# Kernel optimization log

Measured on AMD Instinct MI355X. Metric: run time of the kernel, lower is better.

Reference implementation:

```python
import jax, jax.numpy as jnp
import numpy as np

S = 100                     # MC weight samples
B = 128                     # batch
CONV1 = (100, 20, 1, 5, 5)  # (S, Cout, Cin, kh, kw)
CONV2 = (100, 50, 20, 5, 5)
AFF1 = (100, 500, 800)      # (S, out, in)
AFF2 = (100, 10, 500)
W_OFF = np.cumsum([0, 500, 25000, 400000, 5000])
B_OFF = np.cumsum([0, 20, 50, 500, 10])
NW, NB = 430500, 580


def _softplus(r):
    return jnp.log1p(jnp.exp(r))  # sigma_T(rho) = log(1 + exp(rho))


def _conv(h, w, b):
    # h: (B, S or 1, Cin, H, W); w: (S, Cout, Cin, kh, kw); b: (S, Cout)
    def one(xs, ws):  # xs: (B,Cin,H,W), ws: (Cout,Cin,kh,kw)
        return jax.lax.conv_general_dilated(xs, ws, (1, 1), 'VALID')
    if h.shape[1] == 1:  # shared input broadcast over samples (first layer)
        out = jax.vmap(one, in_axes=(None, 0), out_axes=1)(h[:, 0], w)
    else:
        out = jax.vmap(one, in_axes=(1, 0), out_axes=1)(h, w)
    return out + b[None, :, :, None, None]  # (B,S,Cout,H',W')


def _maxpool(h):  # 2x2 stride-2 over trailing spatial dims
    return jax.lax.reduce_window(h, -jnp.inf, jax.lax.max,
                                 (1, 1, 1, 2, 2), (1, 1, 1, 2, 2), 'VALID')


def setup_inputs() -> dict:
    key = jax.random.key(0)
    ks = jax.random.split(key, 4)
    x = jax.random.normal(ks[0], (B, 1, 28, 28), dtype=jnp.float32)
    e = jax.random.normal(ks[1], (S, NW + NB), dtype=jnp.float32)
    mu_w = jax.random.normal(ks[2], (NW,), dtype=jnp.float32) * 0.05
    rho_w = jnp.ones((NW,), dtype=jnp.float32) * 0.5
    mu_b = jax.random.normal(ks[3], (NB,), dtype=jnp.float32) * 0.05
    rho_b = jnp.ones((NB,), dtype=jnp.float32) * 0.5
    return {"x": x, "e": e, "mu_w": mu_w, "rho_w": rho_w,
            "mu_b": mu_b, "rho_b": rho_b}


def reference(x, e, mu_w, rho_w, mu_b, rho_b):
    # reparameterized per-sample weights: (S, NW) and (S, NB)
    w = mu_w + _softplus(rho_w) * e[:, :NW]
    b = mu_b + _softplus(rho_b) * e[:, NW:]

    h = x[:, None]  # (B,1,1,28,28): singleton MC dim broadcasts
    # conv1 + relu + pool
    h = _conv(h, w[:, W_OFF[0]:W_OFF[1]].reshape(CONV1), b[:, B_OFF[0]:B_OFF[1]])
    h = _maxpool(jax.nn.relu(h))                     # (B,S,20,12,12)
    # conv2 + relu + pool
    h = _conv(h, w[:, W_OFF[1]:W_OFF[2]].reshape(CONV2), b[:, B_OFF[1]:B_OFF[2]])
    h = _maxpool(jax.nn.relu(h))                     # (B,S,50,4,4)
    h = h.reshape(h.shape[0], h.shape[1], -1)        # (B,S,800)
    # aff1 + relu
    w3 = w[:, W_OFF[2]:W_OFF[3]].reshape(AFF1)
    h = jax.nn.relu(jnp.einsum('bsi,soi->bso', h, w3) + b[None, :, B_OFF[2]:B_OFF[3]])
    # aff2 + log_softmax
    w4 = w[:, W_OFF[3]:W_OFF[4]].reshape(AFF2)
    h = jnp.einsum('bsi,soi->bso', h, w4) + b[None, :, B_OFF[3]:B_OFF[4]]
    h = jax.nn.log_softmax(h, axis=-1)               # (B,S,10)
    return h.mean(axis=1)                            # eval path: mean over MC samples
```

## Files before the change

kernel.cpp:

```cpp
#include <hip/hip_runtime.h>
#include <math.h>

#define Sn 100
#define Bn 128
#define NWc 430500
#define EWc 431080

typedef __attribute__((ext_vector_type(8)))  short bhalf8;
typedef __attribute__((ext_vector_type(16))) float fx16;

__device__ __forceinline__ float sp_f(float r){
    return fmaxf(r, 0.f) + log1pf(__expf(-fabsf(r)));
}
__device__ __forceinline__ ushort bfr(float f){
    union { float f; uint u; } c; c.f = f;
    uint r = (c.u + 0x7FFFu + ((c.u >> 16) & 1u)) >> 16;
    return (ushort)r;
}

__global__ void k00_sp(const float* __restrict__ rho_w, const float* __restrict__ rho_b,
                       float* __restrict__ sp_all){
    int i = blockIdx.x * blockDim.x + threadIdx.x;
    if (i < NWc)      sp_all[i] = sp_f(rho_w[i]);
    else if (i < EWc) sp_all[i] = sp_f(rho_b[i - NWc]);
}

__global__ void k0_gen(const float* __restrict__ e, const float* __restrict__ mu_w,
                       const float* __restrict__ sp_all, const float* __restrict__ mu_b,
                       float* __restrict__ w1, ushort* __restrict__ w2r,
                       float* __restrict__ w4, float* __restrict__ ball){
    const int per = 31080;
    int idx = blockIdx.x * blockDim.x + threadIdx.x;
    if (idx >= Sn * per) return;
    int s = idx / per, j = idx % per;
    if (j < 500){
        float v = fmaf(sp_all[j], e[s*EWc + j], mu_w[j]);
        w1[s*500 + j] = v;
    } else if (j < 25500){
        int g = j;
        float v = fmaf(sp_all[g], e[s*EWc + g], mu_w[g]);
        int j2 = j - 500;
        int oc = j2 / 500, rem = j2 % 500;
        int ic = rem / 25, kk = rem % 25;
        w2r[s*51200 + (kk*64 + oc)*32 + ic] = bfr(v);
    } else if (j < 30500){
        int g = 425500 + (j - 25500);
        float v = fmaf(sp_all[g], e[s*EWc + g], mu_w[g]);
        w4[s*5000 + (j - 25500)] = v;
    } else {
        int k = j - 30500;
        float v = fmaf(sp_all[NWc + k], e[s*EWc + NWc + k], mu_b[k]);
        ball[s*580 + k] = v;
    }
}

__global__ __launch_bounds__(256, 2) void k1_conv1(const float* __restrict__ x,
        const float* __restrict__ w1, const float* __restrict__ ball,
        ushort* __restrict__ h1p){
    __shared__ __align__(16) float xs[784];
    __shared__ __align__(16) float w1s[500];
    __shared__ float b1s[20];
    __shared__ __align__(16) ushort ots[2880];
    int bid = blockIdx.x;
    int s = bid / Bn, b = bid % Bn;
    int tid = threadIdx.x;
    for (int i = tid; i < 784; i += 256) xs[i] = x[b*784 + i];
    for (int i = tid; i < 500; i += 256) w1s[i] = w1[s*500 + i];
    if (tid < 20) b1s[tid] = ball[s*580 + tid];
    __syncthreads();
    if (tid < 240){
        int c = tid / 12, y = tid % 12;

        float acc0[24], acc1[24];
        #pragma unroll
        for (int i = 0; i < 24; ++i){ acc0[i] = 0.f; acc1[i] = 0.f; }

        #pragma unroll
        for (int ky = 0; ky < 5; ++ky){
            float rlo[28], rhi[28];
            const float* plo = &xs[(2*y + ky) * 28];
            const float* phi = &xs[(2*y + ky + 1) * 28];
            #pragma unroll
            for (int cc = 0; cc < 28; cc += 4){
                float4 v0 = *(const float4*)(plo + cc);
                rlo[cc] = v0.x; rlo[cc+1] = v0.y; rlo[cc+2] = v0.z; rlo[cc+3] = v0.w;
                float4 v1 = *(const float4*)(phi + cc);
                rhi[cc] = v1.x; rhi[cc+1] = v1.y; rhi[cc+2] = v1.z; rhi[cc+3] = v1.w;
            }
            #pragma unroll
            for (int kx = 0; kx < 5; ++kx){
                float wv = w1s[c*25 + ky*5 + kx];
                #pragma unroll
                for (int cx = 0; cx < 24; ++cx){
                    acc0[cx] = fmaf(rlo[cx + kx], wv, acc0[cx]);
                    acc1[cx] = fmaf(rhi[cx + kx], wv, acc1[cx]);
                }
            }
        }
        float bias = b1s[c];
        #pragma unroll
        for (int px = 0; px < 12; ++px){
            float m = fmaxf(fmaxf(acc0[2*px], acc0[2*px+1]),
                            fmaxf(acc1[2*px], acc1[2*px+1]));
            ots[(y*12 + px)*20 + c] = bfr(fmaxf(m + bias, 0.f));
        }
    }
    __syncthreads();
    const uint* o32 = (const uint*)ots;
    uint* g32 = (uint*)(h1p + (s*Bn + b)*2880);
    for (int j = tid; j < 1440; j += 256) g32[j] = o32[j];
}

#define ICS 40
__global__ __launch_bounds__(256, 3) void k2_mfma(const ushort* __restrict__ h1p,
        const ushort* __restrict__ w2r, const float* __restrict__ ball,
        ushort* __restrict__ h2p){
    __shared__ __align__(16) ushort img[4*144*ICS];
    __shared__ __align__(16) ushort Bs[64*ICS];
    int bid = blockIdx.x;
    int s = bid >> 5, g = bid & 31;
    int tid = threadIdx.x;
    const uint* g32 = (const uint*)(h1p + (size_t)(s*Bn + g*4)*2880);
    uint* l32 = (uint*)img;
    for (int j = tid; j < 5760; j += 256){
        int im = j / 1440, r = j - im*1440;
        int p = r / 10, u = r - p*10;
        l32[im*2880 + p*20 + u] = g32[j];
    }
    for (int j = tid; j < 3456; j += 256){
        int im = j / 864, r = j - im*864;
        int p = r / 6, u = 10 + (r - p*6);
        l32[im*2880 + p*20 + u] = 0u;
    }
    int wv = tid >> 6, l = tid & 63;
    int l31 = l & 31, q = l >> 5;
    const ushort* imgw = img + wv*5760;
    int pixb0 = ((l31      ) >> 3)*12 + (l31 & 7);
    int pixb1 = ((l31 + 32 ) >> 3)*12 + (l31 & 7);
    fx16 acc00 = (fx16)0.f, acc01 = (fx16)0.f, acc10 = (fx16)0.f, acc11 = (fx16)0.f;

    for (int kk = 0; kk < 25; ++kk){
        __syncthreads();
        {
            uint4 v = ((const uint4*)(w2r + (size_t)(s*25 + kk)*2048))[tid];
            *(uint4*)&Bs[(tid>>2)*ICS + (tid&3)*8] = v;
        }
        __syncthreads();
        int ky = kk / 5, kx = kk - ky*5;
        int poff = ky*12 + kx;
        #pragma unroll
        for (int ics = 0; ics < 2; ++ics){
            bhalf8 a0 = *(const bhalf8*)(imgw + (pixb0 + poff)*ICS + ics*16 + q*8);
            bhalf8 a1 = *(const bhalf8*)(imgw + (pixb1 + poff)*ICS + ics*16 + q*8);
            bhalf8 b0 = *(const bhalf8*)(Bs + (l31     )*ICS + ics*16 + q*8);
            bhalf8 b1 = *(const bhalf8*)(Bs + (l31 + 32)*ICS + ics*16 + q*8);
            acc00 = __builtin_amdgcn_mfma_f32_32x32x16_bf16(a0, b0, acc00, 0, 0, 0);
            acc01 = __builtin_amdgcn_mfma_f32_32x32x16_bf16(a0, b1, acc01, 0, 0, 0);
            acc10 = __builtin_amdgcn_mfma_f32_32x32x16_bf16(a1, b0, acc10, 0, 0, 0);
            acc11 = __builtin_amdgcn_mfma_f32_32x32x16_bf16(a1, b1, acc11, 0, 0, 0);
        }
    }
    int b = g*4 + wv;
    ushort* dst = h2p + (size_t)(s*Bn + b)*800;
    #pragma unroll
    for (int nt = 0; nt < 2; ++nt){
        int oc = nt*32 + l31;
        if (oc >= 50) continue;
        float bias = ball[s*580 + 20 + oc];
        #pragma unroll
        for (int mt = 0; mt < 2; ++mt){
            fx16 a;
            if (nt == 0) a = mt ? acc10 : acc00;
            else         a = mt ? acc11 : acc01;
            #pragma unroll
            for (int gp = 0; gp < 2; ++gp){
                float p0 = fmaxf(fmaxf(a[8*gp+0], a[8*gp+1]), fmaxf(a[8*gp+4], a[8*gp+5]));
                float p1 = fmaxf(fmaxf(a[8*gp+2], a[8*gp+3]), fmaxf(a[8*gp+6], a[8*gp+7]));
                p0 = fmaxf(p0 + bias, 0.f);
                p1 = fmaxf(p1 + bias, 0.f);
                int py = mt*2 + gp, px0 = 2*q;
                uint pk = (uint)bfr(p0) | ((uint)bfr(p1) << 16);
                *(uint*)(dst + oc*16 + py*4 + px0) = pk;
            }
        }
    }
}

__global__ __launch_bounds__(256) void k3_mfma(const ushort* __restrict__ h2p,
        const float* __restrict__ e, const float* __restrict__ mu_w,
        const float* __restrict__ sp_all, const float* __restrict__ ball,
        float* __restrict__ h3){
    __shared__ __align__(16) ushort As[128*ICS];
    __shared__ __align__(16) ushort Bsh[64*ICS];
    int bid = blockIdx.x;
    int s = bid >> 3, nblk = bid & 7;
    int o0 = nblk * 64;
    int tid = threadIdx.x;
    int wv = tid >> 6, l = tid & 63, l31 = l & 31, q = l >> 5;
    int wm = wv >> 1, wn = wv & 1;
    fx16 acc0 = (fx16)0.f, acc1 = (fx16)0.f;
    int sb = tid >> 1, sh = tid & 1;
    int so = tid >> 2, sk = (tid & 3)*8;
    int og = o0 + so;
    bool bvalid = og < 500;
    const float* mp = mu_w   + 25500 + og*800 + sk;
    const float* pp = sp_all + 25500 + og*800 + sk;
    const float* ep = e + (size_t)s*EWc + 25500 + og*800 + sk;
    const ushort* ap = h2p + (size_t)(s*Bn + sb)*800 + sh*16;

    uint4 ar0, ar1;
    float4 mva, mvb, sva, svb, eva, evb;
    ar0 = ((const uint4*)ap)[0]; ar1 = ((const uint4*)ap)[1];
    if (bvalid){
        mva = *(const float4*)(mp);   mvb = *(const float4*)(mp + 4);
        sva = *(const float4*)(pp);   svb = *(const float4*)(pp + 4);
        eva = *(const float4*)(ep);   evb = *(const float4*)(ep + 4);
    }

    for (int k0 = 0; k0 < 800; k0 += 32){
        __syncthreads();
        *(uint4*)&As[sb*ICS + sh*16]     = ar0;
        *(uint4*)&As[sb*ICS + sh*16 + 8] = ar1;
        {
            ushort tmp[8];
            if (bvalid){
                tmp[0] = bfr(fmaf(sva.x, eva.x, mva.x));
                tmp[1] = bfr(fmaf(sva.y, eva.y, mva.y));
                tmp[2] = bfr(fmaf(sva.z, eva.z, mva.z));
                tmp[3] = bfr(fmaf(sva.w, eva.w, mva.w));
                tmp[4] = bfr(fmaf(svb.x, evb.x, mvb.x));
                tmp[5] = bfr(fmaf(svb.y, evb.y, mvb.y));
                tmp[6] = bfr(fmaf(svb.z, evb.z, mvb.z));
                tmp[7] = bfr(fmaf(svb.w, evb.w, mvb.w));
            } else {
                #pragma unroll
                for (int j2 = 0; j2 < 8; ++j2) tmp[j2] = 0;
            }
            *(uint4*)&Bsh[so*ICS + sk] = *(const uint4*)tmp;
        }
        __syncthreads();
        int kn = k0 + 32;
        if (kn < 800){
            ar0 = ((const uint4*)(ap + kn))[0]; ar1 = ((const uint4*)(ap + kn))[1];
            if (bvalid){
                mva = *(const float4*)(mp + kn);  mvb = *(const float4*)(mp + kn + 4);
                sva = *(const float4*)(pp + kn);  svb = *(const float4*)(pp + kn + 4);
                eva = *(const float4*)(ep + kn);  evb = *(const float4*)(ep + kn + 4);
            }
        }
        #pragma unroll
        for (int ks = 0; ks < 2; ++ks){
            bhalf8 a0 = *(const bhalf8*)&As[(wm*64      + l31)*ICS + ks*16 + q*8];
            bhalf8 a1 = *(const bhalf8*)&As[(wm*64 + 32 + l31)*ICS + ks*16 + q*8];
            bhalf8 bb = *(const bhalf8*)&Bsh[(wn*32 + l31)*ICS + ks*16 + q*8];
            acc0 = __builtin_amdgcn_mfma_f32_32x32x16_bf16(a0, bb, acc0, 0, 0, 0);
            acc1 = __builtin_amdgcn_mfma_f32_32x32x16_bf16(a1, bb, acc1, 0, 0, 0);
        }
    }
    int o = o0 + wn*32 + l31;
    if (o < 500){
        float bias = ball[s*580 + 70 + o];
        #pragma unroll
        for (int mt = 0; mt < 2; ++mt){
            fx16 a = mt ? acc1 : acc0;
            #pragma unroll
            for (int reg = 0; reg < 16; ++reg){
                int row = (reg & 3) + 8*(reg >> 2) + 4*q;
                int b = wm*64 + mt*32 + row;
                h3[(size_t)(s*Bn + b)*500 + o] = fmaxf(a[reg] + bias, 0.f);
            }
        }
    }
}

__global__ __launch_bounds__(256) void k4a(const float* __restrict__ h3,
        const float* __restrict__ w4, const float* __restrict__ ball,
        float* __restrict__ lsw){
    int wv = threadIdx.x >> 6, lane = threadIdx.x & 63;
    int p = blockIdx.x*4 + wv;
    int s = p / Bn;
    const float* hp = &h3[(size_t)p*500];
    const float* wp = &w4[(size_t)s*5000];
    float part[10];
    #pragma unroll
    for (int o = 0; o < 10; ++o) part[o] = 0.f;
    for (int i = lane; i < 500; i += 64){
        float hv = hp[i];
        #pragma unroll
        for (int o = 0; o < 10; ++o)
            part[o] = fmaf(hv, wp[o*500 + i], part[o]);
    }
    #pragma unroll
    for (int o = 0; o < 10; ++o){
        #pragma unroll
        for (int d = 1; d < 64; d <<= 1)
            part[o] += __shfl_xor(part[o], d);
    }
    float v[10]; float m = -INFINITY;
    #pragma unroll
    for (int o = 0; o < 10; ++o){
        v[o] = part[o] + ball[s*580 + 570 + o];
        m = fmaxf(m, v[o]);
    }
    float sum = 0.f;
    #pragma unroll
    for (int o = 0; o < 10; ++o) sum += __expf(v[o] - m);
    float lse = m + __logf(sum);
    if (lane == 0){
        #pragma unroll
        for (int o = 0; o < 10; ++o) lsw[p*10 + o] = v[o] - lse;
    }
}

__global__ void k4b(const float* __restrict__ lsw, float* __restrict__ outp){
    int j = blockIdx.x * blockDim.x + threadIdx.x;
    if (j >= Bn*10) return;
    int b = j / 10, o = j % 10;
    float acc = 0.f;
    for (int s2 = 0; s2 < Sn; ++s2) acc += lsw[(s2*Bn + b)*10 + o];
    outp[j] = acc * (1.f / (float)Sn);
}

extern "C" void kernel_launch(void* const* d_in, const int* in_sizes, int n_in,
                              void* d_out, int out_size, void* d_ws, size_t ws_size,
                              hipStream_t stream){
    const float* x     = (const float*)d_in[0];
    const float* e     = (const float*)d_in[1];
    const float* mu_w  = (const float*)d_in[2];
    const float* rho_w = (const float*)d_in[3];
    const float* mu_b  = (const float*)d_in[4];
    const float* rho_b = (const float*)d_in[5];
    float* ws   = (float*)d_ws;
    float* w1     = ws;
    float* w4     = w1 + 50000;
    float* ball   = w4 + 500000;
    float* h3     = ball + 58000;
    float* lsw    = h3 + 6400000;
    float* sp_all = lsw + 128000;
    ushort* h1p = (ushort*)(sp_all + 431080);
    ushort* h2p = h1p + 36864000;
    ushort* w2r = h2p + 10240000;
    float* outp = (float*)d_out;

    hipMemsetAsync(w2r, 0, (size_t)Sn*51200*2, stream);
    k00_sp  <<<(EWc + 255)/256, 256, 0, stream>>>(rho_w, rho_b, sp_all);
    k0_gen  <<<(Sn*31080 + 255)/256, 256, 0, stream>>>(e, mu_w, sp_all, mu_b, w1, w2r, w4, ball);
    k1_conv1<<<Sn*Bn, 256, 0, stream>>>(x, w1, ball, h1p);
    k2_mfma <<<Sn*32, 256, 0, stream>>>(h1p, w2r, ball, h2p);
    k3_mfma <<<Sn*8, 256, 0, stream>>>(h2p, e, mu_w, sp_all, ball, h3);
    k4a     <<<3200, 256, 0, stream>>>(h3, w4, ball, lsw);
    k4b     <<<(Bn*10 + 255)/256, 256, 0, stream>>>(lsw, outp);
}
```

Before: 566.5 us.

## Load MFMA B operands directly from global memory in conv2 and aff1 kernels

Both the conv2 and aff1 MFMA kernels stop staging weight and activation tiles through shared memory. Each lane now loads its MFMA fragments straight from global memory, which removes the per-iteration __syncthreads barriers and LDS round-trips. In aff1, each wave recomputes the reparameterized weights for its own columns, so global and L2 traffic goes up: operands that used to be shared across waves are now loaded separately by each wave. An unused bias LDS array is also added to conv2.

```diff
diff --git a/kernel.cpp b/kernel.cpp
--- a/kernel.cpp
+++ b/kernel.cpp
@@ -112,11 +112,11 @@
 }
 
 #define ICS 40
-__global__ __launch_bounds__(256, 3) void k2_mfma(const ushort* __restrict__ h1p,
+__global__ __launch_bounds__(256, 3) void k2_direct(const ushort* __restrict__ h1p,
         const ushort* __restrict__ w2r, const float* __restrict__ ball,
         ushort* __restrict__ h2p){
     __shared__ __align__(16) ushort img[4*144*ICS];
-    __shared__ __align__(16) ushort Bs[64*ICS];
+    __shared__ float b2s[50];
     int bid = blockIdx.x;
     int s = bid >> 5, g = bid & 31;
     int tid = threadIdx.x;
@@ -132,34 +132,34 @@
         int p = r / 6, u = 10 + (r - p*6);
         l32[im*2880 + p*20 + u] = 0u;
     }
+    __syncthreads();
+
     int wv = tid >> 6, l = tid & 63;
     int l31 = l & 31, q = l >> 5;
     const ushort* imgw = img + wv*5760;
     int pixb0 = ((l31      ) >> 3)*12 + (l31 & 7);
     int pixb1 = ((l31 + 32 ) >> 3)*12 + (l31 & 7);
+    const ushort* wb0 = w2r + (size_t)(s*25)*2048 + (l31     )*32;
+    const ushort* wb1 = w2r + (size_t)(s*25)*2048 + (l31 + 32)*32;
     fx16 acc00 = (fx16)0.f, acc01 = (fx16)0.f, acc10 = (fx16)0.f, acc11 = (fx16)0.f;
 
+    #pragma unroll 1
     for (int kk = 0; kk < 25; ++kk){
-        __syncthreads();
-        {
-            uint4 v = ((const uint4*)(w2r + (size_t)(s*25 + kk)*2048))[tid];
-            *(uint4*)&Bs[(tid>>2)*ICS + (tid&3)*8] = v;
-        }
-        __syncthreads();
         int ky = kk / 5, kx = kk - ky*5;
         int poff = ky*12 + kx;
         #pragma unroll
         for (int ics = 0; ics < 2; ++ics){
             bhalf8 a0 = *(const bhalf8*)(imgw + (pixb0 + poff)*ICS + ics*16 + q*8);
             bhalf8 a1 = *(const bhalf8*)(imgw + (pixb1 + poff)*ICS + ics*16 + q*8);
-            bhalf8 b0 = *(const bhalf8*)(Bs + (l31     )*ICS + ics*16 + q*8);
-            bhalf8 b1 = *(const bhalf8*)(Bs + (l31 + 32)*ICS + ics*16 + q*8);
+            bhalf8 b0 = *(const bhalf8*)(wb0 + kk*2048 + ics*16 + q*8);
+            bhalf8 b1 = *(const bhalf8*)(wb1 + kk*2048 + ics*16 + q*8);
             acc00 = __builtin_amdgcn_mfma_f32_32x32x16_bf16(a0, b0, acc00, 0, 0, 0);
             acc01 = __builtin_amdgcn_mfma_f32_32x32x16_bf16(a0, b1, acc01, 0, 0, 0);
             acc10 = __builtin_amdgcn_mfma_f32_32x32x16_bf16(a1, b0, acc10, 0, 0, 0);
             acc11 = __builtin_amdgcn_mfma_f32_32x32x16_bf16(a1, b1, acc11, 0, 0, 0);
         }
     }
+    if (tid < 50) b2s[tid] = ball[s*580 + 20 + tid];
     int b = g*4 + wv;
     ushort* dst = h2p + (size_t)(s*Bn + b)*800;
     #pragma unroll
@@ -186,80 +186,56 @@
     }
 }
 
-__global__ __launch_bounds__(256) void k3_mfma(const ushort* __restrict__ h2p,
+__global__ __launch_bounds__(256) void k3_direct(const ushort* __restrict__ h2p,
         const float* __restrict__ e, const float* __restrict__ mu_w,
         const float* __restrict__ sp_all, const float* __restrict__ ball,
         float* __restrict__ h3){
-    __shared__ __align__(16) ushort As[128*ICS];
-    __shared__ __align__(16) ushort Bsh[64*ICS];
     int bid = blockIdx.x;
     int s = bid >> 3, nblk = bid & 7;
     int o0 = nblk * 64;
     int tid = threadIdx.x;
     int wv = tid >> 6, l = tid & 63, l31 = l & 31, q = l >> 5;
     int wm = wv >> 1, wn = wv & 1;
+    int ob = o0 + wn*32 + l31;
+    bool nv = ob < 500;
+    const ushort* a0p = h2p + (size_t)(s*Bn + wm*64      + l31)*800;
+    const ushort* a1p = h2p + (size_t)(s*Bn + wm*64 + 32 + l31)*800;
+    const float* mp = mu_w   + 25500 + (size_t)ob*800;
+    const float* pp = sp_all + 25500 + (size_t)ob*800;
+    const float* ep = e + (size_t)s*EWc + 25500 + (size_t)ob*800;
     fx16 acc0 = (fx16)0.f, acc1 = (fx16)0.f;
-    int sb = tid >> 1, sh = tid & 1;
-    int so = tid >> 2, sk = (tid & 3)*8;
-    int og = o0 + so;
-    bool bvalid = og < 500;
-    const float* mp = mu_w   + 25500 + og*800 + sk;
-    const float* pp = sp_all + 25500 + og*800 + sk;
-    const float* ep = e + (size_t)s*EWc + 25500 + og*800 + sk;
-    const ushort* ap = h2p + (size_t)(s*Bn + sb)*800 + sh*16;
-
-    uint4 ar0, ar1;
-    float4 mva, mvb, sva, svb, eva, evb;
-    ar0 = ((const uint4*)ap)[0]; ar1 = ((const uint4*)ap)[1];
-    if (bvalid){
-        mva = *(const float4*)(mp);   mvb = *(const float4*)(mp + 4);
-        sva = *(const float4*)(pp);   svb = *(const float4*)(pp + 4);
-        eva = *(const float4*)(ep);   evb = *(const float4*)(ep + 4);
-    }
-
+
+    #pragma unroll 2
     for (int k0 = 0; k0 < 800; k0 += 32){
-        __syncthreads();
-        *(uint4*)&As[sb*ICS + sh*16]     = ar0;
-        *(uint4*)&As[sb*ICS + sh*16 + 8] = ar1;
-        {
-            ushort tmp[8];
-            if (bvalid){
-                tmp[0] = bfr(fmaf(sva.x, eva.x, mva.x));
-                tmp[1] = bfr(fmaf(sva.y, eva.y, mva.y));
-                tmp[2] = bfr(fmaf(sva.z, eva.z, mva.z));
-                tmp[3] = bfr(fmaf(sva.w, eva.w, mva.w));
-                tmp[4] = bfr(fmaf(svb.x, evb.x, mvb.x));
-                tmp[5] = bfr(fmaf(svb.y, evb.y, mvb.y));
-                tmp[6] = bfr(fmaf(svb.z, evb.z, mvb.z));
-                tmp[7] = bfr(fmaf(svb.w, evb.w, mvb.w));
+        #pragma unroll
+        for (int ks = 0; ks < 2; ++ks){
+            int kof = k0 + ks*16 + q*8;
+            bhalf8 av0 = *(const bhalf8*)(a0p + kof);
+            bhalf8 av1 = *(const bhalf8*)(a1p + kof);
+            ushort t[8];
+            if (nv){
+                float4 ev0 = *(const float4*)(ep + kof), ev1 = *(const float4*)(ep + kof + 4);
+                float4 mv0 = *(const float4*)(mp + kof), mv1 = *(const float4*)(mp + kof + 4);
+                float4 sv0 = *(const float4*)(pp + kof), sv1 = *(const float4*)(pp + kof + 4);
+                t[0] = bfr(fmaf(sv0.x, ev0.x, mv0.x));
+                t[1] = bfr(fmaf(sv0.y, ev0.y, mv0.y));
+                t[2] = bfr(fmaf(sv0.z, ev0.z, mv0.z));
+                t[3] = bfr(fmaf(sv0.w, ev0.w, mv0.w));
+                t[4] = bfr(fmaf(sv1.x, ev1.x, mv1.x));
+                t[5] = bfr(fmaf(sv1.y, ev1.y, mv1.y));
+                t[6] = bfr(fmaf(sv1.z, ev1.z, mv1.z));
+                t[7] = bfr(fmaf(sv1.w, ev1.w, mv1.w));
             } else {
                 #pragma unroll
-                for (int j2 = 0; j2 < 8; ++j2) tmp[j2] = 0;
-            }
-            *(uint4*)&Bsh[so*ICS + sk] = *(const uint4*)tmp;
-        }
-        __syncthreads();
-        int kn = k0 + 32;
-        if (kn < 800){
-            ar0 = ((const uint4*)(ap + kn))[0]; ar1 = ((const uint4*)(ap + kn))[1];
-            if (bvalid){
-                mva = *(const float4*)(mp + kn);  mvb = *(const float4*)(mp + kn + 4);
-                sva = *(const float4*)(pp + kn);  svb = *(const float4*)(pp + kn + 4);
-                eva = *(const float4*)(ep + kn);  evb = *(const float4*)(ep + kn + 4);
-            }
-        }
-        #pragma unroll
-        for (int ks = 0; ks < 2; ++ks){
-            bhalf8 a0 = *(const bhalf8*)&As[(wm*64      + l31)*ICS + ks*16 + q*8];
-            bhalf8 a1 = *(const bhalf8*)&As[(wm*64 + 32 + l31)*ICS + ks*16 + q*8];
-            bhalf8 bb = *(const bhalf8*)&Bsh[(wn*32 + l31)*ICS + ks*16 + q*8];
-            acc0 = __builtin_amdgcn_mfma_f32_32x32x16_bf16(a0, bb, acc0, 0, 0, 0);
-            acc1 = __builtin_amdgcn_mfma_f32_32x32x16_bf16(a1, bb, acc1, 0, 0, 0);
-        }
-    }
-    int o = o0 + wn*32 + l31;
-    if (o < 500){
-        float bias = ball[s*580 + 70 + o];
+                for (int j2 = 0; j2 < 8; ++j2) t[j2] = 0;
+            }
+            bhalf8 bb = *(const bhalf8*)t;
+            acc0 = __builtin_amdgcn_mfma_f32_32x32x16_bf16(av0, bb, acc0, 0, 0, 0);
+            acc1 = __builtin_amdgcn_mfma_f32_32x32x16_bf16(av1, bb, acc1, 0, 0, 0);
+        }
+    }
+    if (nv){
+        float bias = ball[s*580 + 70 + ob];
         #pragma unroll
         for (int mt = 0; mt < 2; ++mt){
             fx16 a = mt ? acc1 : acc0;
@@ -267,7 +243,7 @@
             for (int reg = 0; reg < 16; ++reg){
                 int row = (reg & 3) + 8*(reg >> 2) + 4*q;
                 int b = wm*64 + mt*32 + row;
-                h3[(size_t)(s*Bn + b)*500 + o] = fmaxf(a[reg] + bias, 0.f);
+                h3[(size_t)(s*Bn + b)*500 + ob] = fmaxf(a[reg] + bias, 0.f);
             }
         }
     }
@@ -343,11 +319,11 @@
     float* outp = (float*)d_out;
 
     hipMemsetAsync(w2r, 0, (size_t)Sn*51200*2, stream);
-    k00_sp  <<<(EWc + 255)/256, 256, 0, stream>>>(rho_w, rho_b, sp_all);
-    k0_gen  <<<(Sn*31080 + 255)/256, 256, 0, stream>>>(e, mu_w, sp_all, mu_b, w1, w2r, w4, ball);
-    k1_conv1<<<Sn*Bn, 256, 0, stream>>>(x, w1, ball, h1p);
-    k2_mfma <<<Sn*32, 256, 0, stream>>>(h1p, w2r, ball, h2p);
-    k3_mfma <<<Sn*8, 256, 0, stream>>>(h2p, e, mu_w, sp_all, ball, h3);
-    k4a     <<<3200, 256, 0, stream>>>(h3, w4, ball, lsw);
-    k4b     <<<(Bn*10 + 255)/256, 256, 0, stream>>>(lsw, outp);
-}
+    k00_sp   <<<(EWc + 255)/256, 256, 0, stream>>>(rho_w, rho_b, sp_all);
+    k0_gen   <<<(Sn*31080 + 255)/256, 256, 0, stream>>>(e, mu_w, sp_all, mu_b, w1, w2r, w4, ball);
+    k1_conv1 <<<Sn*Bn, 256, 0, stream>>>(x, w1, ball, h1p);
+    k2_direct<<<Sn*32, 256, 0, stream>>>(h1p, w2r, ball, h2p);
+    k3_direct<<<Sn*8, 256, 0, stream>>>(h2p, e, mu_w, sp_all, ball, h3);
+    k4a      <<<3200, 256, 0, stream>>>(h3, w4, ball, lsw);
+    k4b      <<<(Bn*10 + 255)/256, 256, 0, stream>>>(lsw, outp);
+}
```

Measured after the change: 681.8 us. +20.4%, slower.
